# Performance work log

Hardware: AMD Instinct MI355X
Metric: run time of the kernel (lower is better)

The kernel has to match this reference:

```python
import jax, jax.numpy as jnp
import numpy as np

N = 12000   # nodes (multiple of 120)
E = 192000  # edges
T = 120     # utterances per dialogue
IN = 192
OUT = 6


def _edge_softmax(logits, dst, n):
    # logits: [E, H] -> softmax over incoming edges of each dst node
    m = jax.ops.segment_max(logits, dst, num_segments=n)
    ex = jnp.exp(logits - m[dst])
    s = jax.ops.segment_sum(ex, dst, num_segments=n)
    return ex / s[dst]


def _gatv2(h, src, dst, Wsrc, bsrc, Wdst, bdst, attn, Wres, n):
    # DGL GATv2Conv: e = attn . leakyrelu(fc_src(h)[u] + fc_dst(h)[v]), residual, relu activation
    Hh, F = attn.shape
    fs = (h @ Wsrc + bsrc).reshape(n, Hh, F)
    fd = (h @ Wdst + bdst).reshape(n, Hh, F)
    e = jax.nn.leaky_relu(fs[src] + fd[dst], 0.2)          # [E, H, F]
    logits = jnp.einsum('ehf,hf->eh', e, attn)              # [E, H]
    alpha = _edge_softmax(logits, dst, n)                   # [E, H]
    out = jax.ops.segment_sum(alpha[:, :, None] * fs[src], dst, num_segments=n)
    res = (h @ Wres).reshape(n, Hh, F)
    return jax.nn.relu(out + res)                           # [N, H, F]


def _lstm_dir(x, Wih, Whh, bih, bhh, reverse):
    # x: [T, B, D]; torch gate order i, f, g, o
    B = x.shape[1]
    hid = Whh.shape[1]
    def step(carry, xt):
        h, c = carry
        z = xt @ Wih.T + h @ Whh.T + bih + bhh
        i, f, g, o = jnp.split(z, 4, axis=-1)
        c = jax.nn.sigmoid(f) * c + jax.nn.sigmoid(i) * jnp.tanh(g)
        h = jax.nn.sigmoid(o) * jnp.tanh(c)
        return (h, c), h
    init = (jnp.zeros((B, hid), x.dtype), jnp.zeros((B, hid), x.dtype))
    _, hs = jax.lax.scan(step, init, x, reverse=reverse)
    return hs


def setup_inputs() -> dict:
    key = jax.random.key(0)
    ks = iter(jax.random.split(key, 64))
    def rn(shape, s=0.05):
        return jax.random.normal(next(ks), shape, jnp.float32) * s
    inp = {
        'text': rn((N, 1024), 1.0),
        'audio': rn((N, 512), 1.0),
        'vision': rn((N, 1024), 1.0),
        'edge_src': jax.random.randint(next(ks), (E,), 0, N, jnp.int32),
        'edge_dst': jax.random.randint(next(ks), (E,), 0, N, jnp.int32),
        # modality encoders
        'W_audio': rn((512, 64)), 'b_audio': jnp.zeros((64,), jnp.float32),
        'W_vision': rn((1024, 64)), 'b_vision': jnp.zeros((64,), jnp.float32),
        'W_text': rn((1024, 64)), 'b_text': jnp.zeros((64,), jnp.float32),
        # bidirectional LSTM (hidden=4 -> 16 gate rows)
        'Wih_f': rn((16, IN)), 'Whh_f': rn((16, 4)), 'bih_f': jnp.zeros((16,), jnp.float32), 'bhh_f': jnp.zeros((16,), jnp.float32),
        'Wih_b': rn((16, IN)), 'Whh_b': rn((16, 4)), 'bih_b': jnp.zeros((16,), jnp.float32), 'bhh_b': jnp.zeros((16,), jnp.float32),
        # imputation GraphConv (192->192, norm='both')
        'W_gc': rn((IN, IN)), 'b_gc': jnp.zeros((IN,), jnp.float32),
        # gat2 (cross-modal multi-head GAT, 192 -> 16 heads x 4)
        'Wsrc2': rn((IN, 64)), 'bsrc2': jnp.zeros((64,), jnp.float32),
        'Wdst2': rn((IN, 64)), 'bdst2': jnp.zeros((64,), jnp.float32),
        'attn2': rn((16, 4)), 'Wres2': rn((IN, 64)),
        # gat1 layer 0 (192 -> 16 heads x 32)
        'Wsrc0': rn((IN, 512)), 'bsrc0': jnp.zeros((512,), jnp.float32),
        'Wdst0': rn((IN, 512)), 'bdst0': jnp.zeros((512,), jnp.float32),
        'attn0': rn((16, 32)), 'Wres0': rn((IN, 512)),
        # gat1 layer 1 (512 -> 16 heads x 4)
        'Wsrc1': rn((512, 64)), 'bsrc1': jnp.zeros((64,), jnp.float32),
        'Wdst1': rn((512, 64)), 'bdst1': jnp.zeros((64,), jnp.float32),
        'attn1': rn((16, 4)), 'Wres1': rn((512, 64)),
        # final classifier Linear(136, out_size)
        'W_lin': rn((136, OUT)), 'b_lin': jnp.zeros((OUT,), jnp.float32),
    }
    return inp


def reference(text, audio, vision, edge_src, edge_dst,
              W_audio, b_audio, W_vision, b_vision, W_text, b_text,
              Wih_f, Whh_f, bih_f, bhh_f, Wih_b, Whh_b, bih_b, bhh_b,
              W_gc, b_gc,
              Wsrc2, bsrc2, Wdst2, bdst2, attn2, Wres2,
              Wsrc0, bsrc0, Wdst0, bdst0, attn0, Wres0,
              Wsrc1, bsrc1, Wdst1, bdst1, attn1, Wres1,
              W_lin, b_lin):
    n = text.shape[0]
    # modality encoders (dropout is identity at inference)
    t = text @ W_text + b_text
    a = audio @ W_audio + b_audio
    v = vision @ W_vision + b_vision
    stackFT = jnp.concatenate([t, a, v], axis=1)            # [N, 192]

    # bidirectional LSTM over dialogues of length T=120
    x = stackFT.reshape(-1, T, IN).transpose(1, 0, 2)       # [T, B, 192]
    hf = _lstm_dir(x, Wih_f, Whh_f, bih_f, bhh_f, False)
    hb = _lstm_dir(x, Wih_b, Whh_b, bih_b, bhh_b, True)
    newFeature = jnp.concatenate([hf, hb], -1).transpose(1, 0, 2).reshape(n, 8)

    # GraphConv imputation, norm='both' (degrees clamped to 1 as in DGL)
    ones = jnp.ones((edge_src.shape[0],), stackFT.dtype)
    deg_out = jnp.maximum(jax.ops.segment_sum(ones, edge_src, num_segments=n), 1.0)
    deg_in = jnp.maximum(jax.ops.segment_sum(ones, edge_dst, num_segments=n), 1.0)
    hw = (stackFT @ W_gc) * (deg_out ** -0.5)[:, None]
    h1 = jax.ops.segment_sum(hw[edge_src], edge_dst, num_segments=n) * (deg_in ** -0.5)[:, None] + b_gc
    h = 0.5 * (stackFT + h1)
    # F.normalize(h, p=1)
    h = h / jnp.maximum(jnp.sum(jnp.abs(h), axis=1, keepdims=True), 1e-12)

    # cross-modal multi-head GAT branch -> [N, 64]
    h3 = _gatv2(h, edge_src, edge_dst, Wsrc2, bsrc2, Wdst2, bdst2, attn2, Wres2, n).reshape(n, -1)

    # stacked GATv2 layers
    h = _gatv2(h, edge_src, edge_dst, Wsrc0, bsrc0, Wdst0, bdst0, attn0, Wres0, n).reshape(n, -1)  # [N, 512]
    h = _gatv2(h, edge_src, edge_dst, Wsrc1, bsrc1, Wdst1, bdst1, attn1, Wres1, n).reshape(n, -1)  # [N, 64]

    out = jnp.concatenate([h, newFeature, h3], axis=1) @ W_lin + b_lin  # [N, out_size]
    return out
```

## Files before the change

### kernel.cpp

```cpp
#include <hip/hip_runtime.h>

typedef __attribute__((ext_vector_type(8))) short short8;
typedef __attribute__((ext_vector_type(4))) float f32x4;
typedef _Float16 half8v __attribute__((ext_vector_type(8)));

__device__ __forceinline__ unsigned short f2bf(float f) {
    unsigned u = __float_as_uint(f);
    u += 0x7FFFu + ((u >> 16) & 1u);
    return (unsigned short)(u >> 16);
}
__device__ __forceinline__ float bf2f(unsigned short h) {
    return __uint_as_float((unsigned)h << 16);
}

template<int MF, int OUTMODE>
__global__ __launch_bounds__(256)
void gemm_v7(const unsigned short* __restrict__ A, const unsigned short* __restrict__ B,
             const float* __restrict__ bias, const float* __restrict__ rowscale,
             void* __restrict__ Cv, const float* __restrict__ fin_num,
             const float* __restrict__ fin_den,
             int M, int Nb, int K, int ldc)
{
    __shared__ alignas(16) unsigned short As[MF * 64 * 32];
    __shared__ alignas(16) unsigned short Bs[4 * 64 * 8];
    const int t = threadIdx.x;
    const int w = t >> 6, l = t & 63;
    const int r16 = l & 15, kg = l >> 4;
    const int row0 = blockIdx.x * (64 * MF);
    const int col0 = blockIdx.y * 64;
    const int bcol = t & 63, bkg = t >> 6;

    f32x4 acc[MF][4] = {};
    const short8 z8 = {0, 0, 0, 0, 0, 0, 0, 0};

    int srow[MF], sch[MF];
    bool va[MF];
    const unsigned short* aptr[MF];
#pragma unroll
    for (int it = 0; it < MF; ++it) {
        int idx = it * 256 + t;
        srow[it] = idx >> 2; sch[it] = idx & 3;
        int gm = row0 + srow[it];
        va[it] = gm < M;
        aptr[it] = A + (size_t)gm * K + sch[it] * 8;
    }
    const unsigned short* bptr = B + (size_t)(bkg * 8) * Nb + col0 + bcol;

    short8 pa[MF];
    unsigned short pbv[8];
#pragma unroll
    for (int it = 0; it < MF; ++it)
        pa[it] = va[it] ? *reinterpret_cast<const short8*>(aptr[it]) : z8;
#pragma unroll
    for (int j = 0; j < 8; ++j) pbv[j] = bptr[(size_t)j * Nb];

    for (int k0 = 0; k0 < K; k0 += 32) {
#pragma unroll
        for (int it = 0; it < MF; ++it)
            *reinterpret_cast<short8*>(&As[srow[it] * 32 + sch[it] * 8]) = pa[it];
        {
            short8 hv;
#pragma unroll
            for (int j = 0; j < 8; ++j) hv[j] = (short)pbv[j];
            *reinterpret_cast<short8*>(&Bs[bkg * 512 + bcol * 8]) = hv;
        }
        __syncthreads();
        if (k0 + 32 < K) {
#pragma unroll
            for (int it = 0; it < MF; ++it)
                pa[it] = va[it] ? *reinterpret_cast<const short8*>(aptr[it] + k0 + 32) : z8;
#pragma unroll
            for (int j = 0; j < 8; ++j) pbv[j] = bptr[(size_t)(k0 + 32 + j) * Nb];
        }
        short8 af[MF];
#pragma unroll
        for (int mi = 0; mi < MF; ++mi)
            af[mi] = *reinterpret_cast<const short8*>(&As[((w * MF + mi) * 16 + r16) * 32 + kg * 8]);
#pragma unroll
        for (int ni = 0; ni < 4; ++ni) {
            short8 bf = *reinterpret_cast<const short8*>(&Bs[kg * 512 + (ni * 16 + r16) * 8]);
#pragma unroll
            for (int mi = 0; mi < MF; ++mi)
                acc[mi][ni] = __builtin_amdgcn_mfma_f32_16x16x32_bf16(af[mi], bf, acc[mi][ni], 0, 0, 0);
        }
        __syncthreads();
    }
#pragma unroll
    for (int mi = 0; mi < MF; ++mi)
#pragma unroll
        for (int ni = 0; ni < 4; ++ni) {
            int col = col0 + ni * 16 + r16;
            float bv = bias ? bias[col] : 0.f;
#pragma unroll
            for (int r = 0; r < 4; ++r) {
                int gm = row0 + (w * MF + mi) * 16 + kg * 4 + r;
                if (gm < M) {
                    float val = acc[mi][ni][r] + bv;
                    if (rowscale) val *= rowscale[gm];
                    size_t idx = (size_t)gm * ldc + col;
                    if (OUTMODE == 0) {
                        ((float*)Cv)[idx] = val;
                    } else if (OUTMODE == 1) {
                        ((unsigned short*)Cv)[idx] = f2bf(val);
                    } else if (OUTMODE == 2) {
                        float d = fin_den[(size_t)gm * 16 + (col >> 5)];
                        float inv = (d > 0.f) ? __fdividef(1.f, d) : 0.f;
                        float o = fmaxf(fin_num[idx] * inv + val, 0.f);
                        ((unsigned short*)Cv)[idx] = f2bf(o);
                    } else {
                        if (col < 32) {
                            int d = col >> 4, j = col & 15;
                            int bb = gm / 120, tt = gm - bb * 120;
                            float* dst = d ? (float*)fin_num : (float*)Cv;
                            dst[((size_t)bb * 16 + j) * 120 + tt] = val;
                        }
                    }
                }
            }
        }
}

__global__ __launch_bounds__(256)
void enc_f16v6(const float* __restrict__ text, const float* __restrict__ audio, const float* __restrict__ vision,
               const _Float16* __restrict__ Wf16,
               const float* __restrict__ bt, const float* __restrict__ ba, const float* __restrict__ bv,
               float* __restrict__ Cf, unsigned short* __restrict__ Cb, int M)
{
    __shared__ float tbuf[4][16][68];
    const int gw = (blockIdx.x * blockDim.x + threadIdx.x) >> 6;
    const int wib = threadIdx.x >> 6;
    const int l = threadIdx.x & 63;
    const int tpm = M >> 4;
    if (gw >= 3 * tpm) return;
    const int z = gw / tpm;
    const int tidx = gw - z * tpm;
    const float* A  = (z == 0) ? text : (z == 1) ? audio : vision;
    const _Float16* Wp = Wf16 + ((z == 0) ? 0 : (z == 1) ? 65536 : 98304) + l * 8;
    const float* bb = (z == 0) ? bt : (z == 1) ? ba : bv;
    const int KC = (z == 1) ? 16 : 32;

    const float* ap = A + (size_t)(tidx * 16 + (l & 15)) * (KC * 32) + (l >> 4) * 8;

    f32x4 acc0 = {}, acc1 = {}, acc2 = {}, acc3 = {};
    float4 na0 = *reinterpret_cast<const float4*>(ap);
    float4 na1 = *reinterpret_cast<const float4*>(ap + 4);
    half8v nb0 = *reinterpret_cast<const half8v*>(Wp);
    half8v nb1 = *reinterpret_cast<const half8v*>(Wp + 512);
    half8v nb2 = *reinterpret_cast<const half8v*>(Wp + 1024);
    half8v nb3 = *reinterpret_cast<const half8v*>(Wp + 1536);

    for (int kc = 0; kc < KC; ++kc) {
        float4 ca0 = na0, ca1 = na1;
        half8v cb0 = nb0, cb1 = nb1, cb2 = nb2, cb3 = nb3;
        if (kc + 1 < KC) {
            const float* apn = ap + (kc + 1) * 32;
            na0 = *reinterpret_cast<const float4*>(apn);
            na1 = *reinterpret_cast<const float4*>(apn + 4);
            const _Float16* wpn = Wp + (size_t)(kc + 1) * 2048;
            nb0 = *reinterpret_cast<const half8v*>(wpn);
            nb1 = *reinterpret_cast<const half8v*>(wpn + 512);
            nb2 = *reinterpret_cast<const half8v*>(wpn + 1024);
            nb3 = *reinterpret_cast<const half8v*>(wpn + 1536);
        }
        half8v af;
        af[0] = (_Float16)ca0.x; af[1] = (_Float16)ca0.y;
        af[2] = (_Float16)ca0.z; af[3] = (_Float16)ca0.w;
        af[4] = (_Float16)ca1.x; af[5] = (_Float16)ca1.y;
        af[6] = (_Float16)ca1.z; af[7] = (_Float16)ca1.w;
        acc0 = __builtin_amdgcn_mfma_f32_16x16x32_f16(af, cb0, acc0, 0, 0, 0);
        acc1 = __builtin_amdgcn_mfma_f32_16x16x32_f16(af, cb1, acc1, 0, 0, 0);
        acc2 = __builtin_amdgcn_mfma_f32_16x16x32_f16(af, cb2, acc2, 0, 0, 0);
        acc3 = __builtin_amdgcn_mfma_f32_16x16x32_f16(af, cb3, acc3, 0, 0, 0);
    }

    const int r16 = l & 15, hi = l >> 4;
    float* tl = &tbuf[wib][0][0];
#pragma unroll
    for (int cg = 0; cg < 4; ++cg) {
        f32x4 a = (cg == 0) ? acc0 : (cg == 1) ? acc1 : (cg == 2) ? acc2 : acc3;
        int col = cg * 16 + r16;
        float bvv = bb[col];
#pragma unroll
        for (int r = 0; r < 4; ++r)
            tl[(hi * 4 + r) * 68 + col] = a[r] + bvv;
    }
#pragma unroll
    for (int r = 0; r < 16; ++r) {
        float val = tl[r * 68 + l];
        size_t idx = (size_t)(tidx * 16 + r) * 192 + z * 64 + l;
        Cf[idx] = val;
        Cb[idx] = f2bf(val);
    }
}

__global__ void pack_all(const float* __restrict__ Wt, const float* __restrict__ Wa, const float* __restrict__ Wv,
                         const float* __restrict__ Wgc,
                         const float* __restrict__ Ws2, const float* __restrict__ Wd2, const float* __restrict__ Wr2,
                         const float* __restrict__ bs2, const float* __restrict__ bd2,
                         const float* __restrict__ Ws0, const float* __restrict__ Wd0,
                         const float* __restrict__ bs0, const float* __restrict__ bd0,
                         const float* __restrict__ Wr0,
                         const float* __restrict__ Ws1, const float* __restrict__ Wd1, const float* __restrict__ Wr1,
                         const float* __restrict__ bs1, const float* __restrict__ bd1,
                         const float* __restrict__ Wihf, const float* __restrict__ Wihb,
                         const float* __restrict__ bihf, const float* __restrict__ bhhf,
                         const float* __restrict__ bihb, const float* __restrict__ bhhb,
                         _Float16* __restrict__ encW, unsigned short* __restrict__ Wall, float* __restrict__ ball)
{
    int gid = blockIdx.x * blockDim.x + threadIdx.x;
    if (gid < 163840) {
        const float* Wsrcp;
        int base;
        if (gid < 65536)      { base = 0;     Wsrcp = Wt; }
        else if (gid < 98304) { base = 65536; Wsrcp = Wa; }
        else                  { base = 98304; Wsrcp = Wv; }
        int i = gid - base;
        int kc = i >> 11, r = i & 2047;
        int cg = r >> 9, lane = (r >> 3) & 63, j = r & 7;
        int k = kc * 32 + (lane >> 4) * 8 + j;
        int col = cg * 16 + (lane & 15);
        encW[gid] = (_Float16)Wsrcp[k * 64 + col];
    }
    if (gid < 36864) {
        Wall[gid] = f2bf(Wgc[gid]);
    } else if (gid < 73728) {
        int i = gid - 36864, k = i / 192, c = i - k * 192;
        float v = (c < 64) ? Ws2[k * 64 + c] : (c < 128) ? Wd2[k * 64 + c - 64] : Wr2[k * 64 + c - 128];
        Wall[gid] = f2bf(v);
    } else if (gid < 270336) {
        int i = gid - 73728, k = i >> 10, c = i & 1023;
        float v = (c < 512) ? Ws0[k * 512 + c] : Wd0[k * 512 + c - 512];
        Wall[gid] = f2bf(v);
    } else if (gid < 368640) {
        Wall[gid] = f2bf(Wr0[gid - 270336]);
    } else if (gid < 466944) {
        int i = gid - 368640, k = i / 192, c = i - k * 192;
        float v = (c < 64) ? Ws1[k * 64 + c] : (c < 128) ? Wd1[k * 64 + c - 64] : Wr1[k * 64 + c - 128];
        Wall[gid] = f2bf(v);
    } else if (gid < 479232) {
        int i = gid - 466944, k = i >> 6, c = i & 63;
        float v = (c < 16) ? Wihf[c * 192 + k] : (c < 32) ? Wihb[(c - 16) * 192 + k] : 0.f;
        Wall[gid] = f2bf(v);
    } else if (gid < 480672) {
        int i = gid - 479232;
        float v;
        if (i < 192)       v = (i < 64) ? bs2[i] : (i < 128) ? bd2[i - 64] : 0.f;
        else if (i < 1216) { int j = i - 192; v = (j < 512) ? bs0[j] : bd0[j - 512]; }
        else if (i < 1408) { int j = i - 1216; v = (j < 64) ? bs1[j] : (j < 128) ? bd1[j - 64] : 0.f; }
        else               { int j = i - 1408; v = (j < 16) ? (bihf[j] + bhhf[j]) : (bihb[j - 16] + bhhb[j - 16]); }
        ball[i] = v;
    }
}

__global__ void deg_kernel(const int* __restrict__ src, const int* __restrict__ dst,
                           int* degout, int* degin, int E)
{
    int e = blockIdx.x * blockDim.x + threadIdx.x;
    if (e < E) {
        atomicAdd(&degout[src[e]], 1);
        atomicAdd(&degin[dst[e]], 1);
    }
}

__global__ __launch_bounds__(1024)
void scan_kernel(const int* __restrict__ degin, const int* __restrict__ degout,
                 int* __restrict__ rowstart, float* __restrict__ rso, float* __restrict__ rsi, int n)
{
    __shared__ int part[1024];
    int t = threadIdx.x;
    int chunk = (n + 1023) / 1024;
    int s = 0;
    for (int i = 0; i < chunk; ++i) {
        int idx = t * chunk + i;
        if (idx < n) s += degin[idx];
    }
    part[t] = s;
    __syncthreads();
    for (int o = 1; o < 1024; o <<= 1) {
        int v = (t >= o) ? part[t - o] : 0;
        __syncthreads();
        part[t] += v;
        __syncthreads();
    }
    int run = (t > 0) ? part[t - 1] : 0;
    for (int i = 0; i < chunk; ++i) {
        int idx = t * chunk + i;
        if (idx < n) {
            rowstart[idx] = run; run += degin[idx];
            rso[idx] = rsqrtf((float)max(degout[idx], 1));
            rsi[idx] = rsqrtf((float)max(degin[idx], 1));
        }
    }
    if (t == 1023) rowstart[n] = part[1023];
}

__global__ void perm_kernel(const int* __restrict__ dst, const int* __restrict__ rowstart,
                            int* cursor, int* __restrict__ perm, int E)
{
    int e = blockIdx.x * blockDim.x + threadIdx.x;
    if (e < E) {
        int v = dst[e];
        int p = atomicAdd(&cursor[v], 1);
        perm[rowstart[v] + p] = e;
    }
}

__global__ void gather_src_kernel(const int* __restrict__ esrc, int* perm, int E)
{
    int i = blockIdx.x * blockDim.x + threadIdx.x;
    if (i < E) perm[i] = esrc[perm[i]];
}

__device__ __forceinline__ float fsigm(float x) { return __fdividef(1.f, 1.f + __expf(-x)); }
__device__ __forceinline__ float ftanh(float x) { return 1.f - __fdividef(2.f, __expf(2.f * x) + 1.f); }

template<int DIR>
__device__ void lstm_chain(const float* __restrict__ xw, const float* __restrict__ whh,
                           float* __restrict__ newF, int b)
{
    int j = threadIdx.x & 15;
    int k = j & 3;
    float4 w = *reinterpret_cast<const float4*>(whh + j * 4);
    const float* xp = xw + ((size_t)b * 16 + j) * 120;
    float h0 = 0.f, h1 = 0.f, h2 = 0.f, h3 = 0.f, cst = 0.f;
    int tb0 = DIR ? 108 : 0;
    float4 a0 = *reinterpret_cast<const float4*>(xp + tb0);
    float4 a1 = *reinterpret_cast<const float4*>(xp + tb0 + 4);
    float4 a2 = *reinterpret_cast<const float4*>(xp + tb0 + 8);
    for (int ch = 0; ch < 10; ++ch) {
        float4 b0 = a0, b1 = a1, b2 = a2;
        if (ch < 9) {
            int nt = DIR ? (96 - ch * 12) : (12 + ch * 12);
            b0 = *reinterpret_cast<const float4*>(xp + nt);
            b1 = *reinterpret_cast<const float4*>(xp + nt + 4);
            b2 = *reinterpret_cast<const float4*>(xp + nt + 8);
        }
        float zz[12] = {a0.x, a0.y, a0.z, a0.w, a1.x, a1.y, a1.z, a1.w, a2.x, a2.y, a2.z, a2.w};
        int tbase = DIR ? (108 - ch * 12) : (ch * 12);
#pragma unroll
        for (int ii = 0; ii < 12; ++ii) {
            int idx = DIR ? (11 - ii) : ii;
            float z = zz[idx] + ((w.x * h0 + w.y * h1) + (w.z * h2 + w.w * h3));
            float zi = __shfl(z, k, 16);
            float zf = __shfl(z, k + 4, 16);
            float zg = __shfl(z, k + 8, 16);
            float zo = __shfl(z, k + 12, 16);
            float ig = fsigm(zi), fg = fsigm(zf), gg = ftanh(zg), og = fsigm(zo);
            cst = fg * cst + ig * gg;
            float hn = og * ftanh(cst);
            h0 = __shfl(hn, 0, 16); h1 = __shfl(hn, 1, 16);
            h2 = __shfl(hn, 2, 16); h3 = __shfl(hn, 3, 16);
            if (j < 4) newF[((size_t)b * 120 + tbase + idx) * 8 + DIR * 4 + j] = hn;
        }
        a0 = b0; a1 = b1; a2 = b2;
    }
}

__global__ __launch_bounds__(64)
void lstm_seq2(const float* __restrict__ xWf, const float* __restrict__ xWb,
               const float* __restrict__ Whhf, const float* __restrict__ Whhb,
               float* __restrict__ newF, int B)
{
    int sub = threadIdx.x >> 4;
    int chain = blockIdx.x * 4 + sub;
    if (chain >= 2 * B) return;
    int d = chain / B;
    int b = chain - d * B;
    if (d == 0) lstm_chain<0>(xWf, Whhf, newF, b);
    else        lstm_chain<1>(xWb, Whhb, newF, b);
}

__global__ __launch_bounds__(256)
void gc_combine5(const float* __restrict__ stackFT, const unsigned short* __restrict__ hw,
                 const int* __restrict__ rowstart, const int* __restrict__ csrc,
                 const float* __restrict__ rs_in,
                 const float* __restrict__ b_gc, unsigned short* __restrict__ hB, int n)
{
    int v = blockIdx.x * 4 + (threadIdx.x >> 6);
    int l = threadIdx.x & 63;
    if (v >= n) return;
    int s0 = rowstart[v], s1 = rowstart[v + 1];
    float sum0 = 0.f, sum1 = 0.f, sum2 = 0.f;

    unsigned short a0 = 0, a1 = 0, a2 = 0, b0 = 0, b1 = 0, b2 = 0;
    auto LD = [&](int i, unsigned short& x0, unsigned short& x1, unsigned short& x2) {
        const unsigned short* hr = hw + (size_t)csrc[i] * 192 + l;
        x0 = hr[0]; x1 = hr[64]; x2 = hr[128];
    };
    int i = s0;
    if (i < s1) LD(i, a0, a1, a2);
    if (i + 1 < s1) LD(i + 1, b0, b1, b2);
    for (; i + 2 < s1; i += 2) {
        unsigned short n0, n1, n2, m0 = 0, m1 = 0, m2 = 0;
        LD(i + 2, n0, n1, n2);
        if (i + 3 < s1) LD(i + 3, m0, m1, m2);
        sum0 += bf2f(a0) + bf2f(b0);
        sum1 += bf2f(a1) + bf2f(b1);
        sum2 += bf2f(a2) + bf2f(b2);
        a0 = n0; a1 = n1; a2 = n2; b0 = m0; b1 = m1; b2 = m2;
    }
    if (i < s1) { sum0 += bf2f(a0); sum1 += bf2f(a1); sum2 += bf2f(a2); }
    if (i + 1 < s1) { sum0 += bf2f(b0); sum1 += bf2f(b1); sum2 += bf2f(b2); }

    float ri = rs_in[v];
    const float* sf = stackFT + (size_t)v * 192 + l;
    float v0 = 0.5f * (sf[0]   + sum0 * ri + b_gc[l]);
    float v1 = 0.5f * (sf[64]  + sum1 * ri + b_gc[l + 64]);
    float v2 = 0.5f * (sf[128] + sum2 * ri + b_gc[l + 128]);
    float r = fabsf(v0) + fabsf(v1) + fabsf(v2);
#pragma unroll
    for (int o = 32; o; o >>= 1) r += __shfl_xor(r, o);
    float inv = __fdividef(1.f, fmaxf(r, 1e-12f));
    unsigned short* hp = hB + (size_t)v * 192 + l;
    hp[0]   = f2bf(v0 * inv);
    hp[64]  = f2bf(v1 * inv);
    hp[128] = f2bf(v2 * inv);
}

__global__ __launch_bounds__(256)
void gat_edge4c(const unsigned short* __restrict__ base,
                const float* __restrict__ attn,
                const int* __restrict__ rowstart, const int* __restrict__ csrc,
                float* __restrict__ outp, int n)
{
    int v = blockIdx.x * 16 + (threadIdx.x >> 4);
    int l = threadIdx.x & 15;
    if (v >= n) return;
    float4 at = *reinterpret_cast<const float4*>(attn + l * 4);
    ushort4 fdu = *reinterpret_cast<const ushort4*>(base + (size_t)v * 192 + 64 + l * 4);
    float fd0 = bf2f(fdu.x), fd1 = bf2f(fdu.y), fd2 = bf2f(fdu.z), fd3 = bf2f(fdu.w);
    float ac0 = 0.f, ac1 = 0.f, ac2 = 0.f, ac3 = 0.f, dn = 0.f;
    int s0 = rowstart[v], s1 = rowstart[v + 1];

    auto LD = [&](int i) -> ushort4 {
        return *reinterpret_cast<const ushort4*>(base + (size_t)csrc[i] * 192 + l * 4);
    };
    auto ACC = [&](ushort4 su) {
        float s0f = bf2f(su.x), s1f = bf2f(su.y), s2f = bf2f(su.z), s3f = bf2f(su.w);
        float e0 = s0f + fd0; e0 = fmaxf(e0, 0.2f * e0);
        float e1 = s1f + fd1; e1 = fmaxf(e1, 0.2f * e1);
        float e2 = s2f + fd2; e2 = fmaxf(e2, 0.2f * e2);
        float e3 = s3f + fd3; e3 = fmaxf(e3, 0.2f * e3);
        float p = e0 * at.x + e1 * at.y + e2 * at.z + e3 * at.w;
        float ex = __expf(p);
        ac0 += ex * s0f; ac1 += ex * s1f; ac2 += ex * s2f; ac3 += ex * s3f;
        dn += ex;
    };
    const ushort4 zu = make_ushort4(0, 0, 0, 0);
    ushort4 c0 = zu, c1 = zu, c2 = zu, c3 = zu;
    int i = s0;
    if (i     < s1) c0 = LD(i);
    if (i + 1 < s1) c1 = LD(i + 1);
    if (i + 2 < s1) c2 = LD(i + 2);
    if (i + 3 < s1) c3 = LD(i + 3);
    for (; i + 4 < s1; i += 4) {
        ushort4 n0 = LD(i + 4);
        ushort4 n1 = (i + 5 < s1) ? LD(i + 5) : zu;
        ushort4 n2 = (i + 6 < s1) ? LD(i + 6) : zu;
        ushort4 n3 = (i + 7 < s1) ? LD(i + 7) : zu;
        ACC(c0); ACC(c1); ACC(c2); ACC(c3);
        c0 = n0; c1 = n1; c2 = n2; c3 = n3;
    }
    if (i     < s1) ACC(c0);
    if (i + 1 < s1) ACC(c1);
    if (i + 2 < s1) ACC(c2);
    if (i + 3 < s1) ACC(c3);

    ushort4 ru = *reinterpret_cast<const ushort4*>(base + (size_t)v * 192 + 128 + l * 4);
    float inv = (dn > 0.f) ? __fdividef(1.f, dn) : 0.f;
    float4 o;
    o.x = fmaxf(ac0 * inv + bf2f(ru.x), 0.f);
    o.y = fmaxf(ac1 * inv + bf2f(ru.y), 0.f);
    o.z = fmaxf(ac2 * inv + bf2f(ru.z), 0.f);
    o.w = fmaxf(ac3 * inv + bf2f(ru.w), 0.f);
    *reinterpret_cast<float4*>(outp + (size_t)v * 64 + l * 4) = o;
}

__global__ __launch_bounds__(256)
void gat_edge32b(const unsigned short* __restrict__ base,
                 const float* __restrict__ attn,
                 const int* __restrict__ rowstart, const int* __restrict__ csrc,
                 float* __restrict__ num, float* __restrict__ den, int n)
{
    int v = blockIdx.x * 4 + (threadIdx.x >> 6);
    int l = threadIdx.x & 63;
    if (v >= n) return;
    float at[8];
    {
        float4 aA = *reinterpret_cast<const float4*>(attn + l * 8);
        float4 aB = *reinterpret_cast<const float4*>(attn + l * 8 + 4);
        at[0] = aA.x; at[1] = aA.y; at[2] = aA.z; at[3] = aA.w;
        at[4] = aB.x; at[5] = aB.y; at[6] = aB.z; at[7] = aB.w;
    }
    float fd[8];
    {
        short8 fdu = *reinterpret_cast<const short8*>(base + (size_t)v * 1024 + 512 + l * 8);
#pragma unroll
        for (int j = 0; j < 8; ++j) fd[j] = bf2f((unsigned short)fdu[j]);
    }
    float acc[8] = {};
    float dn = 0.f;
    int s0 = rowstart[v], s1 = rowstart[v + 1];

    auto LD = [&](int i) -> short8 {
        return *reinterpret_cast<const short8*>(base + (size_t)csrc[i] * 1024 + l * 8);
    };
    auto ACC = [&](short8 su) {
        float sf[8];
        float p = 0.f;
#pragma unroll
        for (int j = 0; j < 8; ++j) {
            sf[j] = bf2f((unsigned short)su[j]);
            float e = sf[j] + fd[j];
            e = fmaxf(e, 0.2f * e);
            p += e * at[j];
        }
        p += __shfl_xor(p, 1, 4);
        p += __shfl_xor(p, 2, 4);
        float ex = __expf(p);
#pragma unroll
        for (int j = 0; j < 8; ++j) acc[j] += ex * sf[j];
        dn += ex;
    };
    const short8 z8 = {0, 0, 0, 0, 0, 0, 0, 0};
    short8 c0 = z8, c1 = z8, c2 = z8, c3 = z8;
    int i = s0;
    if (i     < s1) c0 = LD(i);
    if (i + 1 < s1) c1 = LD(i + 1);
    if (i + 2 < s1) c2 = LD(i + 2);
    if (i + 3 < s1) c3 = LD(i + 3);
    for (; i + 4 < s1; i += 4) {
        short8 n0 = LD(i + 4);
        short8 n1 = (i + 5 < s1) ? LD(i + 5) : z8;
        short8 n2 = (i + 6 < s1) ? LD(i + 6) : z8;
        short8 n3 = (i + 7 < s1) ? LD(i + 7) : z8;
        ACC(c0); ACC(c1); ACC(c2); ACC(c3);
        c0 = n0; c1 = n1; c2 = n2; c3 = n3;
    }
    if (i     < s1) ACC(c0);
    if (i + 1 < s1) ACC(c1);
    if (i + 2 < s1) ACC(c2);
    if (i + 3 < s1) ACC(c3);

    float* np = num + (size_t)v * 512 + l * 8;
    *reinterpret_cast<float4*>(np)     = make_float4(acc[0], acc[1], acc[2], acc[3]);
    *reinterpret_cast<float4*>(np + 4) = make_float4(acc[4], acc[5], acc[6], acc[7]);
    if ((l & 3) == 0) den[(size_t)v * 16 + (l >> 2)] = dn;
}

__global__ void final_lin(const float* __restrict__ h1, const float* __restrict__ newF,
                          const float* __restrict__ h3, const float* __restrict__ W,
                          const float* __restrict__ bias, float* __restrict__ out, int n)
{
    int gid = blockIdx.x * blockDim.x + threadIdx.x;
    if (gid >= n * 6) return;
    int v = gid / 6, o = gid - v * 6;
    float s = bias[o];
    const float* a = h1 + (size_t)v * 64;
#pragma unroll 8
    for (int r = 0; r < 64; ++r) s += a[r] * W[r * 6 + o];
    const float* b = newF + (size_t)v * 8;
#pragma unroll
    for (int r = 0; r < 8; ++r) s += b[r] * W[(64 + r) * 6 + o];
    const float* c = h3 + (size_t)v * 64;
#pragma unroll 8
    for (int r = 0; r < 64; ++r) s += c[r] * W[(72 + r) * 6 + o];
    out[gid] = s;
}

extern "C" void kernel_launch(void* const* d_in, const int* in_sizes, int n_in,
                              void* d_out, int out_size, void* d_ws, size_t ws_size,
                              hipStream_t stream)
{
    const float* text   = (const float*)d_in[0];
    const float* audio  = (const float*)d_in[1];
    const float* vision = (const float*)d_in[2];
    const int*   esrc   = (const int*)d_in[3];
    const int*   edst   = (const int*)d_in[4];
    const float* W_audio = (const float*)d_in[5];  const float* b_audio = (const float*)d_in[6];
    const float* W_vision= (const float*)d_in[7];  const float* b_vision= (const float*)d_in[8];
    const float* W_text  = (const float*)d_in[9];  const float* b_text  = (const float*)d_in[10];
    const float* Wih_f = (const float*)d_in[11]; const float* Whh_f = (const float*)d_in[12];
    const float* bih_f = (const float*)d_in[13]; const float* bhh_f = (const float*)d_in[14];
    const float* Wih_b = (const float*)d_in[15]; const float* Whh_b = (const float*)d_in[16];
    const float* bih_b = (const float*)d_in[17]; const float* bhh_b = (const float*)d_in[18];
    const float* W_gc  = (const float*)d_in[19]; const float* b_gc  = (const float*)d_in[20];
    const float* Wsrc2 = (const float*)d_in[21]; const float* bsrc2 = (const float*)d_in[22];
    const float* Wdst2 = (const float*)d_in[23]; const float* bdst2 = (const float*)d_in[24];
    const float* attn2 = (const float*)d_in[25]; const float* Wres2 = (const float*)d_in[26];
    const float* Wsrc0 = (const float*)d_in[27]; const float* bsrc0 = (const float*)d_in[28];
    const float* Wdst0 = (const float*)d_in[29]; const float* bdst0 = (const float*)d_in[30];
    const float* attn0 = (const float*)d_in[31]; const float* Wres0 = (const float*)d_in[32];
    const float* Wsrc1 = (const float*)d_in[33]; const float* bsrc1 = (const float*)d_in[34];
    const float* Wdst1 = (const float*)d_in[35]; const float* bdst1 = (const float*)d_in[36];
    const float* attn1 = (const float*)d_in[37]; const float* Wres1 = (const float*)d_in[38];
    const float* W_lin = (const float*)d_in[39]; const float* b_lin = (const float*)d_in[40];
    float* out = (float*)d_out;

    const int n = in_sizes[0] / 1024;
    const int E = in_sizes[3];
    const int B = n / 120;

    char* p = (char*)d_ws;
    auto alloc_f = [&](size_t cnt) { float* r = (float*)p; p += ((cnt * 4 + 255) / 256) * 256; return r; };
    auto alloc_h = [&](size_t cnt) { unsigned short* r = (unsigned short*)p; p += ((cnt * 2 + 255) / 256) * 256; return r; };
    auto alloc_i = [&](size_t cnt) { int* r = (int*)p; p += ((cnt * 4 + 255) / 256) * 256; return r; };
    float*          stackFT = alloc_f((size_t)n * 192);
    unsigned short* stackBF = alloc_h((size_t)n * 192);
    unsigned short* hbufBF  = alloc_h((size_t)n * 192);
    unsigned short* encW    = alloc_h(163840);
    float* xWf     = alloc_f((size_t)n * 16);
    float* xWb     = alloc_f((size_t)n * 16);
    float* newF    = alloc_f((size_t)n * 8);
    float* big0    = alloc_f((size_t)n * 512);
    float* big1    = alloc_f((size_t)n * 512);
    float* big2    = alloc_f((size_t)n * 512);
    float* den     = alloc_f((size_t)n * 16);
    float* h3      = alloc_f((size_t)n * 64);
    float* h1s     = alloc_f((size_t)n * 64);
    float* rs_out  = alloc_f(n);
    float* rs_in   = alloc_f(n);
    int* zero_base = alloc_i((size_t)3 * n);
    int* degout = zero_base;
    int* degin  = zero_base + n;
    int* cursor = zero_base + 2 * n;
    int* rowstart = alloc_i((size_t)n + 1);
    int* perm     = alloc_i((size_t)E);
    if ((size_t)(p - (char*)d_ws) > ws_size) return;

    unsigned short* Wall = (unsigned short*)h1s;
    float* ball = h1s + 240000;
    const unsigned short* Wp_gc   = Wall;
    const unsigned short* Wp_g2   = Wall + 36864;
    const unsigned short* Wp_g0   = Wall + 73728;
    const unsigned short* Wp_r0   = Wall + 270336;
    const unsigned short* Wp_g1   = Wall + 368640;
    const unsigned short* Wp_lstm = Wall + 466944;
    const float* bp_g2   = ball;
    const float* bp_g0   = ball + 192;
    const float* bp_g1   = ball + 1216;
    const float* bp_lstm = ball + 1408;

    hipMemsetAsync(zero_base, 0, (size_t)3 * n * 4, stream);
    pack_all<<<(480672 + 255) / 256, 256, 0, stream>>>(
        W_text, W_audio, W_vision, W_gc,
        Wsrc2, Wdst2, Wres2, bsrc2, bdst2,
        Wsrc0, Wdst0, bsrc0, bdst0, Wres0,
        Wsrc1, Wdst1, Wres1, bsrc1, bdst1,
        Wih_f, Wih_b, bih_f, bhh_f, bih_b, bhh_b,
        (_Float16*)encW, Wall, ball);
    deg_kernel<<<(E + 255) / 256, 256, 0, stream>>>(esrc, edst, degout, degin, E);
    scan_kernel<<<1, 1024, 0, stream>>>(degin, degout, rowstart, rs_out, rs_in, n);
    perm_kernel<<<(E + 255) / 256, 256, 0, stream>>>(edst, rowstart, cursor, perm, E);
    gather_src_kernel<<<(E + 255) / 256, 256, 0, stream>>>(esrc, perm, E);
    const int* csrc = perm;

    auto gemm = [&](auto mf_tag, auto om_tag, const unsigned short* A, const unsigned short* Bm,
                    const float* bias, const float* rsc, void* Cp,
                    const float* fnum, const float* fden, int M, int Nb, int K, int ldc) {
        constexpr int MF = decltype(mf_tag)::value;
        constexpr int OM = decltype(om_tag)::value;
        dim3 grid((M + 64 * MF - 1) / (64 * MF), Nb / 64);
        gemm_v7<MF, OM><<<grid, 256, 0, stream>>>(A, Bm, bias, rsc, Cp, fnum, fden, M, Nb, K, ldc);
    };
    using I1 = std::integral_constant<int, 1>;
    using I2 = std::integral_constant<int, 2>;
    using O1 = std::integral_constant<int, 1>;
    using O2 = std::integral_constant<int, 2>;
    using O3 = std::integral_constant<int, 3>;

    {
        int waves = 3 * (n >> 4);
        enc_f16v6<<<(waves * 64 + 255) / 256, 256, 0, stream>>>(
            text, audio, vision, (const _Float16*)encW,
            b_text, b_audio, b_vision, stackFT, stackBF, n);
    }

    gemm(I1{}, O3{}, stackBF, Wp_lstm, bp_lstm, nullptr, xWf, xWb, nullptr, n, 64, 192, 64);
    lstm_seq2<<<(2 * B + 3) / 4, 64, 0, stream>>>(xWf, xWb, Whh_f, Whh_b, newF, B);

    gemm(I1{}, O1{}, stackBF, Wp_gc, nullptr, rs_out, big0, nullptr, nullptr, n, 192, 192, 192);
    gc_combine5<<<(n + 3) / 4, 256, 0, stream>>>(stackFT, (const unsigned short*)big0,
                                                 rowstart, csrc, rs_in, b_gc, hbufBF, n);

    gemm(I1{}, O1{}, hbufBF, Wp_g2, bp_g2, nullptr, big0, nullptr, nullptr, n, 192, 192, 192);
    gat_edge4c<<<(n + 15) / 16, 256, 0, stream>>>((const unsigned short*)big0, attn2, rowstart, csrc, h3, n);

    gemm(I2{}, O1{}, hbufBF, Wp_g0, bp_g0, nullptr, big0, nullptr, nullptr, n, 1024, 192, 1024);
    gat_edge32b<<<(n + 3) / 4, 256, 0, stream>>>((const unsigned short*)big0, attn0, rowstart, csrc, big2, den, n);
    gemm(I1{}, O2{}, hbufBF, Wp_r0, nullptr, nullptr, big1, big2, den, n, 512, 192, 512);

    gemm(I1{}, O1{}, (const unsigned short*)big1, Wp_g1, bp_g1, nullptr, big0, nullptr, nullptr, n, 192, 512, 192);
    gat_edge4c<<<(n + 15) / 16, 256, 0, stream>>>((const unsigned short*)big0, attn1, rowstart, csrc, h1s, n);

    final_lin<<<(n * 6 + 255) / 256, 256, 0, stream>>>(h1s, newF, h3, W_lin, b_lin, out, n);
}
```

Baseline: 331.4 us.

## Split encoder K loop across four waves and fuse degree counting into pack kernel

The encoder kernel now assigns each 16-row tile to a whole 256-thread block and splits the K dimension across its four waves. The partial accumulators are reduced through shared memory before the bias and store epilogue, which gives more parallelism and memory-level concurrency per tile. Separately, the degree-counting atomics move into the weight-packing kernel, removing one kernel launch. The cost is extra LDS traffic, a block barrier, and three idle waves during the epilogue.

After: 327.0 us. About the same (-1.3%).

```diff
diff --git a/kernel.cpp b/kernel.cpp
--- a/kernel.cpp
+++ b/kernel.cpp
@@ -121,25 +121,26 @@
 }
 
 __global__ __launch_bounds__(256)
-void enc_f16v6(const float* __restrict__ text, const float* __restrict__ audio, const float* __restrict__ vision,
+void enc_f16v7(const float* __restrict__ text, const float* __restrict__ audio, const float* __restrict__ vision,
                const _Float16* __restrict__ Wf16,
                const float* __restrict__ bt, const float* __restrict__ ba, const float* __restrict__ bv,
                float* __restrict__ Cf, unsigned short* __restrict__ Cb, int M)
 {
-    __shared__ float tbuf[4][16][68];
-    const int gw = (blockIdx.x * blockDim.x + threadIdx.x) >> 6;
-    const int wib = threadIdx.x >> 6;
-    const int l = threadIdx.x & 63;
+    __shared__ float part[3][16][65];
+    __shared__ float tbuf[16][68];
     const int tpm = M >> 4;
-    if (gw >= 3 * tpm) return;
-    const int z = gw / tpm;
-    const int tidx = gw - z * tpm;
+    const int t3 = blockIdx.x;
+    const int z = t3 / tpm;
+    const int tidx = t3 - z * tpm;
+    const int w = threadIdx.x >> 6, l = threadIdx.x & 63;
     const float* A  = (z == 0) ? text : (z == 1) ? audio : vision;
-    const _Float16* Wp = Wf16 + ((z == 0) ? 0 : (z == 1) ? 65536 : 98304) + l * 8;
+    const _Float16* Wbase = Wf16 + ((z == 0) ? 0 : (z == 1) ? 65536 : 98304);
     const float* bb = (z == 0) ? bt : (z == 1) ? ba : bv;
     const int KC = (z == 1) ? 16 : 32;
-
-    const float* ap = A + (size_t)(tidx * 16 + (l & 15)) * (KC * 32) + (l >> 4) * 8;
+    const int KC4 = KC >> 2;
+
+    const float* ap = A + (size_t)(tidx * 16 + (l & 15)) * (KC * 32) + (l >> 4) * 8 + (size_t)(w * KC4) * 32;
+    const _Float16* Wp = Wbase + l * 8 + (size_t)(w * KC4) * 2048;
 
     f32x4 acc0 = {}, acc1 = {}, acc2 = {}, acc3 = {};
     float4 na0 = *reinterpret_cast<const float4*>(ap);
@@ -149,10 +150,10 @@
     half8v nb2 = *reinterpret_cast<const half8v*>(Wp + 1024);
     half8v nb3 = *reinterpret_cast<const half8v*>(Wp + 1536);
 
-    for (int kc = 0; kc < KC; ++kc) {
+    for (int kc = 0; kc < KC4; ++kc) {
         float4 ca0 = na0, ca1 = na1;
         half8v cb0 = nb0, cb1 = nb1, cb2 = nb2, cb3 = nb3;
-        if (kc + 1 < KC) {
+        if (kc + 1 < KC4) {
             const float* apn = ap + (kc + 1) * 32;
             na0 = *reinterpret_cast<const float4*>(apn);
             na1 = *reinterpret_cast<const float4*>(apn + 4);
@@ -173,23 +174,46 @@
         acc3 = __builtin_amdgcn_mfma_f32_16x16x32_f16(af, cb3, acc3, 0, 0, 0);
     }
 
-    const int r16 = l & 15, hi = l >> 4;
-    float* tl = &tbuf[wib][0][0];
-#pragma unroll
-    for (int cg = 0; cg < 4; ++cg) {
-        f32x4 a = (cg == 0) ? acc0 : (cg == 1) ? acc1 : (cg == 2) ? acc2 : acc3;
-        int col = cg * 16 + r16;
-        float bvv = bb[col];
-#pragma unroll
-        for (int r = 0; r < 4; ++r)
-            tl[(hi * 4 + r) * 68 + col] = a[r] + bvv;
-    }
-#pragma unroll
-    for (int r = 0; r < 16; ++r) {
-        float val = tl[r * 68 + l];
-        size_t idx = (size_t)(tidx * 16 + r) * 192 + z * 64 + l;
-        Cf[idx] = val;
-        Cb[idx] = f2bf(val);
+    if (w > 0) {
+        float* pp = &part[w - 1][0][0];
+#pragma unroll
+        for (int j = 0; j < 4; ++j) {
+            pp[(j)      * 65 + l] = acc0[j];
+            pp[(4 + j)  * 65 + l] = acc1[j];
+            pp[(8 + j)  * 65 + l] = acc2[j];
+            pp[(12 + j) * 65 + l] = acc3[j];
+        }
+    }
+    __syncthreads();
+    if (w == 0) {
+#pragma unroll
+        for (int p = 0; p < 3; ++p) {
+            const float* pp = &part[p][0][0];
+#pragma unroll
+            for (int j = 0; j < 4; ++j) {
+                acc0[j] += pp[(j)      * 65 + l];
+                acc1[j] += pp[(4 + j)  * 65 + l];
+                acc2[j] += pp[(8 + j)  * 65 + l];
+                acc3[j] += pp[(12 + j) * 65 + l];
+            }
+        }
+        const int r16 = l & 15, hi = l >> 4;
+#pragma unroll
+        for (int cg = 0; cg < 4; ++cg) {
+            f32x4 a = (cg == 0) ? acc0 : (cg == 1) ? acc1 : (cg == 2) ? acc2 : acc3;
+            int col = cg * 16 + r16;
+            float bvv = bb[col];
+#pragma unroll
+            for (int r = 0; r < 4; ++r)
+                tbuf[hi * 4 + r][col] = a[r] + bvv;
+        }
+#pragma unroll
+        for (int r = 0; r < 16; ++r) {
+            float val = tbuf[r][l];
+            size_t idx = (size_t)(tidx * 16 + r) * 192 + z * 64 + l;
+            Cf[idx] = val;
+            Cb[idx] = f2bf(val);
+        }
     }
 }
 
@@ -205,9 +229,15 @@
                          const float* __restrict__ Wihf, const float* __restrict__ Wihb,
                          const float* __restrict__ bihf, const float* __restrict__ bhhf,
                          const float* __restrict__ bihb, const float* __restrict__ bhhb,
+                         const int* __restrict__ esrc, const int* __restrict__ edst,
+                         int* degout, int* degin, int E,
                          _Float16* __restrict__ encW, unsigned short* __restrict__ Wall, float* __restrict__ ball)
 {
     int gid = blockIdx.x * blockDim.x + threadIdx.x;
+    if (gid < E) {
+        atomicAdd(&degout[esrc[gid]], 1);
+        atomicAdd(&degin[edst[gid]], 1);
+    }
     if (gid < 163840) {
         const float* Wsrcp;
         int base;
@@ -252,16 +282,6 @@
     }
 }
 
-__global__ void deg_kernel(const int* __restrict__ src, const int* __restrict__ dst,
-                           int* degout, int* degin, int E)
-{
-    int e = blockIdx.x * blockDim.x + threadIdx.x;
-    if (e < E) {
-        atomicAdd(&degout[src[e]], 1);
-        atomicAdd(&degin[dst[e]], 1);
-    }
-}
-
 __global__ __launch_bounds__(1024)
 void scan_kernel(const int* __restrict__ degin, const int* __restrict__ degout,
                  int* __restrict__ rowstart, float* __restrict__ rso, float* __restrict__ rsi, int n)
@@ -648,8 +668,8 @@
         Wsrc0, Wdst0, bsrc0, bdst0, Wres0,
         Wsrc1, Wdst1, Wres1, bsrc1, bdst1,
         Wih_f, Wih_b, bih_f, bhh_f, bih_b, bhh_b,
+        esrc, edst, degout, degin, E,
         (_Float16*)encW, Wall, ball);
-    deg_kernel<<<(E + 255) / 256, 256, 0, stream>>>(esrc, edst, degout, degin, E);
     scan_kernel<<<1, 1024, 0, stream>>>(degin, degout, rowstart, rs_out, rs_in, n);
     perm_kernel<<<(E + 255) / 256, 256, 0, stream>>>(edst, rowstart, cursor, perm, E);
     gather_src_kernel<<<(E + 255) / 256, 256, 0, stream>>>(esrc, perm, E);
@@ -669,12 +689,9 @@
     using O2 = std::integral_constant<int, 2>;
     using O3 = std::integral_constant<int, 3>;
 
-    {
-        int waves = 3 * (n >> 4);
-        enc_f16v6<<<(waves * 64 + 255) / 256, 256, 0, stream>>>(
-            text, audio, vision, (const _Float16*)encW,
-            b_text, b_audio, b_vision, stackFT, stackBF, n);
-    }
+    enc_f16v7<<<3 * (n >> 4), 256, 0, stream>>>(
+        text, audio, vision, (const _Float16*)encW,
+        b_text, b_audio, b_vision, stackFT, stackBF, n);
 
     gemm(I1{}, O3{}, stackBF, Wp_lstm, bp_lstm, nullptr, xWf, xWb, nullptr, n, 64, 192, 64);
     lstm_seq2<<<(2 * B + 3) / 4, 64, 0, stream>>>(xWf, xWb, Whh_f, Whh_b, newF, B);
```
